# Kernel optimization log

Measured on AMD Instinct MI355X. Metric: run time of the kernel, lower is better.

Reference implementation:

```python
import jax, jax.numpy as jnp
import numpy as np

N_NODES = 100000
N_EDGES = 1600000
N_GRAPHS = 1024
HID = 32
EPS = 1e-5


def gcn_conv(x, W, b, row, col):
    # PyG GCNConv: h = x @ W, then symmetric-normalized scatter-add over
    # edges (self-loops already included in row/col).
    h = x @ W  # [N, out]
    deg = jax.ops.segment_sum(jnp.ones_like(col, dtype=h.dtype), col, num_segments=N_NODES)
    dinv = jnp.where(deg > 0, jax.lax.rsqrt(jnp.maximum(deg, 1.0)), 0.0)
    norm = dinv[row] * dinv[col]  # [E+N]
    msg = h[row] * norm[:, None]
    out = jax.ops.segment_sum(msg, col, num_segments=N_NODES)
    return out + b


def graph_norm(x, batch, weight, bias, mean_scale):
    # PyG GraphNorm: per-graph mean/var with learnable mean scale.
    ones = jnp.ones((x.shape[0], 1), dtype=x.dtype)
    cnt = jnp.maximum(jax.ops.segment_sum(ones, batch, num_segments=N_GRAPHS), 1.0)  # [G,1]
    mean = jax.ops.segment_sum(x, batch, num_segments=N_GRAPHS) / cnt
    out = x - mean[batch] * mean_scale
    var = jax.ops.segment_sum(out * out, batch, num_segments=N_GRAPHS) / cnt
    std = jnp.sqrt(var + EPS)
    return weight * out / std[batch] + bias


def setup_inputs() -> dict:
    key = jax.random.key(0)
    ks = jax.random.split(key, 16)
    x = jax.random.normal(ks[0], (N_NODES, 3), dtype=jnp.float32)
    edge_index = jax.random.randint(ks[1], (2, N_EDGES), 0, N_NODES, dtype=jnp.int64)
    batch = jnp.sort(jax.random.randint(ks[2], (N_NODES,), 0, N_GRAPHS, dtype=jnp.int64))
    def lin_init(k, fan_in, shape):
        bound = 1.0 / np.sqrt(fan_in)
        return jax.random.uniform(k, shape, jnp.float32, -bound, bound)
    params = {
        "W1": lin_init(ks[3], 3, (3, HID)), "b1": lin_init(ks[4], 3, (HID,)),
        "W2": lin_init(ks[5], HID, (HID, HID)), "b2": lin_init(ks[6], HID, (HID,)),
        "W3": lin_init(ks[7], HID, (HID, HID)), "b3": lin_init(ks[8], HID, (HID,)),
        "g1": jnp.ones((HID,)), "be1": jnp.zeros((HID,)), "ms1": jnp.ones((HID,)),
        "g2": jnp.ones((HID,)), "be2": jnp.zeros((HID,)), "ms2": jnp.ones((HID,)),
        "g3": jnp.ones((HID,)), "be3": jnp.zeros((HID,)), "ms3": jnp.ones((HID,)),
        "Wl": lin_init(ks[9], HID, (HID, 3)), "bl": lin_init(ks[10], HID, (3,)),
    }
    return {"x": x, "edge_index": edge_index, "batch": batch, **params}


def reference(x, edge_index, batch, W1, b1, W2, b2, W3, b3,
              g1, be1, ms1, g2, be2, ms2, g3, be3, ms3, Wl, bl):
    # Eval mode: dropouts / feature mask / edge dropout are identity.
    loops = jnp.arange(N_NODES, dtype=edge_index.dtype)
    row = jnp.concatenate([edge_index[0], loops])
    col = jnp.concatenate([edge_index[1], loops])

    x1 = jax.nn.relu(graph_norm(gcn_conv(x, W1, b1, row, col), batch, g1, be1, ms1))
    h2 = graph_norm(gcn_conv(x1, W2, b2, row, col), batch, g2, be2, ms2)
    x2 = jax.nn.relu(h2 + x1)
    h3 = graph_norm(gcn_conv(x2, W3, b3, row, col), batch, g3, be3, ms3)
    x3 = jax.nn.relu(h3 + x2)

    pooled = jax.ops.segment_sum(x3, batch, num_segments=N_GRAPHS)  # [G, HID]
    counts = jax.ops.segment_sum(jnp.ones((N_NODES,), jnp.float32), batch, num_segments=N_GRAPHS)
    pooled = pooled / jnp.maximum(counts, 1.0)[:, None]
    return pooled @ Wl + bl  # [G, 3]
```

## Files before the change

kernel.cpp:

```cpp
#include <hip/hip_runtime.h>
#include <hip/hip_fp16.h>


#define NN 100000
#define NE 1600000
#define NG 1024
#define HD 32
#define EPSV 1e-5f

#define FILL_PASSES 4
#define FILL_BLOCKS 2048
#define NPP ((NN + FILL_PASSES - 1) / FILL_PASSES)

__global__ __launch_bounds__(256) void k_bound(const int* __restrict__ batch,
                                               int* __restrict__ gstart) {
    int v = blockIdx.x * 256 + threadIdx.x;
    if (v >= NN) return;
    int b = batch[v];
    int bp = (v > 0) ? batch[v - 1] : -1;
    for (int g = bp + 1; g <= b; g++) gstart[g] = v;
    if (v == NN - 1)
        for (int g = b + 1; g <= NG; g++) gstart[g] = NN;
}

__global__ __launch_bounds__(256) void k_count(const int* __restrict__ col,
                                               int* __restrict__ deg) {
    int e = blockIdx.x * 256 + threadIdx.x;
    if (e < NE) atomicAdd(&deg[col[e]], 1);
}

__global__ __launch_bounds__(256) void k_alloc(const int* __restrict__ deg,
                                               int* __restrict__ start,
                                               float* __restrict__ dinv,
                                               int* __restrict__ counter) {
    int v = blockIdx.x * 256 + threadIdx.x;
    int lane = threadIdx.x & 63;
    int d = (v < NN) ? (deg[v] + 1) : 0;
    int incl = d;
    #pragma unroll
    for (int off = 1; off < 64; off <<= 1) {
        int n = __shfl_up(incl, off);
        if (lane >= off) incl += n;
    }
    int total = __shfl(incl, 63);
    int base = 0;
    if (lane == 63) base = atomicAdd(counter, total);
    base = __shfl(base, 63);
    if (v < NN) {
        start[v] = base + incl - d;
        dinv[v] = rsqrtf((float)d);
    }
}

__global__ __launch_bounds__(256) void k_fill(const int* __restrict__ row,
                                              const int* __restrict__ col,
                                              const int* __restrict__ start,
                                              int* __restrict__ fill,
                                              int* __restrict__ csr_src) {
    const int total = NE + NN;
    const int chunk = (total + FILL_BLOCKS - 1) / FILL_BLOCKS;
    int c0 = blockIdx.x * chunk;
    int c1 = min(c0 + chunk, total);
    for (int pass = 0; pass < FILL_PASSES; pass++) {
        int lo = pass * NPP;
        int hi = lo + NPP;
        for (int e = c0 + threadIdx.x; e < c1; e += 256) {
            int r, c;
            if (e < NE) { r = row[e]; c = col[e]; }
            else        { r = e - NE; c = r; }
            if (c >= lo && c < hi) {
                int pos = start[c] + atomicAdd(&fill[c], 1);
                csr_src[pos] = r;
            }
        }
    }
}

template <int K>
__global__ __launch_bounds__(256) void k_premul(const float* __restrict__ xin,
                                                const float* __restrict__ W,
                                                const float* __restrict__ dinv,
                                                __half* __restrict__ hs) {
    __shared__ float sW[K * HD];
    for (int i = threadIdx.x; i < K * HD; i += 256) sW[i] = W[i];
    __syncthreads();
    int t = blockIdx.x * 256 + threadIdx.x;
    int v = t >> 2, o = t & 3;
    if (v >= NN) return;
    const float* xv = xin + (size_t)v * K;
    float acc[8] = {0.f, 0.f, 0.f, 0.f, 0.f, 0.f, 0.f, 0.f};
    #pragma unroll
    for (int k = 0; k < K; k++) {
        float xk = xv[k];
        #pragma unroll
        for (int j = 0; j < 8; j++) acc[j] += xk * sW[k * HD + o * 8 + j];
    }
    float dv = dinv[v];
    __half2 h[4];
    #pragma unroll
    for (int j = 0; j < 4; j++)
        h[j] = __floats2half2_rn(dv * acc[2 * j], dv * acc[2 * j + 1]);
    *reinterpret_cast<float4*>(hs + (size_t)v * HD + o * 8) = *reinterpret_cast<float4*>(h);
}

__global__ __launch_bounds__(256) void k_gather(const __half* __restrict__ hs,
                                                const int* __restrict__ csr_src,
                                                const int* __restrict__ start,
                                                const int* __restrict__ deg,
                                                const float* __restrict__ dinv,
                                                const float* __restrict__ bias,
                                                float* __restrict__ outb) {
    int wid = (blockIdx.x * 256 + threadIdx.x) >> 6;
    if (wid >= NN) return;
    int lane = threadIdx.x & 63;
    int q = lane & 3;
    int es = lane >> 2;
    int s = start[wid], d = deg[wid] + 1;
    float acc[8] = {0.f, 0.f, 0.f, 0.f, 0.f, 0.f, 0.f, 0.f};

    bool a0 = (es < d);
    bool a1 = (es + 16 < d);
    int src0 = a0 ? csr_src[s + es] : 0;
    int src1 = a1 ? csr_src[s + es + 16] : 0;
    float4 raw0 = *reinterpret_cast<const float4*>(hs + (size_t)src0 * HD + q * 8);
    float4 raw1 = *reinterpret_cast<const float4*>(hs + (size_t)src1 * HD + q * 8);
    float m0 = a0 ? 1.f : 0.f;
    float m1 = a1 ? 1.f : 0.f;
    {
        const __half2* hp = reinterpret_cast<const __half2*>(&raw0);
        #pragma unroll
        for (int j = 0; j < 4; j++) {
            float2 f2 = __half22float2(hp[j]);
            acc[2 * j]     += m0 * f2.x;
            acc[2 * j + 1] += m0 * f2.y;
        }
    }
    {
        const __half2* hp = reinterpret_cast<const __half2*>(&raw1);
        #pragma unroll
        for (int j = 0; j < 4; j++) {
            float2 f2 = __half22float2(hp[j]);
            acc[2 * j]     += m1 * f2.x;
            acc[2 * j + 1] += m1 * f2.y;
        }
    }
    for (int i = es + 32; i < d; i += 16) {
        int src = csr_src[s + i];
        float4 raw = *reinterpret_cast<const float4*>(hs + (size_t)src * HD + q * 8);
        const __half2* hp = reinterpret_cast<const __half2*>(&raw);
        #pragma unroll
        for (int j = 0; j < 4; j++) {
            float2 f2 = __half22float2(hp[j]);
            acc[2 * j]     += f2.x;
            acc[2 * j + 1] += f2.y;
        }
    }
    #pragma unroll
    for (int off = 4; off < 64; off <<= 1) {
        #pragma unroll
        for (int j = 0; j < 8; j++) acc[j] += __shfl_xor(acc[j], off);
    }
    if (es == 0) {
        float dv = dinv[wid];
        float4 w0, w1;
        w0.x = bias[q * 8 + 0] + dv * acc[0];
        w0.y = bias[q * 8 + 1] + dv * acc[1];
        w0.z = bias[q * 8 + 2] + dv * acc[2];
        w0.w = bias[q * 8 + 3] + dv * acc[3];
        w1.x = bias[q * 8 + 4] + dv * acc[4];
        w1.y = bias[q * 8 + 5] + dv * acc[5];
        w1.z = bias[q * 8 + 6] + dv * acc[6];
        w1.w = bias[q * 8 + 7] + dv * acc[7];
        float* op = outb + (size_t)wid * HD + q * 8;
        *reinterpret_cast<float4*>(op)     = w0;
        *reinterpret_cast<float4*>(op + 4) = w1;
    }
}

template <bool RES, bool POOL>
__global__ __launch_bounds__(256) void k_gnorm(const float* __restrict__ o,
                                               const int* __restrict__ gstart,
                                               const float* __restrict__ gamma,
                                               const float* __restrict__ beta,
                                               const float* __restrict__ msc,
                                               const float* __restrict__ xprev,
                                               float* __restrict__ xout,
                                               const float* __restrict__ Wl,
                                               const float* __restrict__ bl,
                                               float* __restrict__ outf) {
    int g = blockIdx.x;
    int s = gstart[g], e = gstart[g + 1];
    int f = threadIdx.x & 31, nl = threadIdx.x >> 5;
    float as = 0.f, aq = 0.f;
    for (int v = s + nl; v < e; v += 8) {
        float xv = o[(size_t)v * HD + f];
        as += xv;
        aq += xv * xv;
    }
    __shared__ float ls[256], lq[256];
    __shared__ float sA[HD], sB[HD];
    ls[threadIdx.x] = as;
    lq[threadIdx.x] = aq;
    __syncthreads();
    if (threadIdx.x < HD) {
        float ss = 0.f, qq = 0.f;
        #pragma unroll
        for (int k = 0; k < 8; k++) { ss += ls[k * 32 + f]; qq += lq[k * 32 + f]; }
        float inv = 1.f / fmaxf((float)(e - s), 1.f);
        float m = ss * inv, mq = qq * inv, ms = msc[f];
        float var = mq - m * m * ms * (2.f - ms);
        float A = gamma[f] * rsqrtf(var + EPSV);
        sA[f] = A;
        sB[f] = beta[f] - A * m * ms;
    }
    __syncthreads();
    float A = sA[f], B = sB[f];
    float pool = 0.f;
    for (int v = s + nl; v < e; v += 8) {
        float xv = o[(size_t)v * HD + f];
        float y = A * xv + B;
        if (RES) y += xprev[(size_t)v * HD + f];
        y = fmaxf(y, 0.f);
        xout[(size_t)v * HD + f] = y;
        if (POOL) pool += y;
    }
    if (POOL) {
        __syncthreads();
        ls[threadIdx.x] = pool;
        __syncthreads();
        if (threadIdx.x < HD) {
            float ss = 0.f;
            #pragma unroll
            for (int k = 0; k < 8; k++) ss += ls[k * 32 + f];
            lq[f] = ss / fmaxf((float)(e - s), 1.f);
        }
        __syncthreads();
        if (threadIdx.x < 3) {
            float acc = bl[threadIdx.x];
            #pragma unroll
            for (int f2 = 0; f2 < HD; f2++) acc += lq[f2] * Wl[f2 * 3 + threadIdx.x];
            outf[g * 3 + threadIdx.x] = acc;
        }
    }
}

extern "C" void kernel_launch(void* const* d_in, const int* in_sizes, int n_in,
                              void* d_out, int out_size, void* d_ws, size_t ws_size,
                              hipStream_t stream) {
    const float* x     = (const float*)d_in[0];
    const int*   ei    = (const int*)d_in[1];
    const int*   batch = (const int*)d_in[2];
    const float* W1 = (const float*)d_in[3];
    const float* b1 = (const float*)d_in[4];
    const float* W2 = (const float*)d_in[5];
    const float* b2 = (const float*)d_in[6];
    const float* W3 = (const float*)d_in[7];
    const float* b3 = (const float*)d_in[8];
    const float* g1 = (const float*)d_in[9];
    const float* be1 = (const float*)d_in[10];
    const float* ms1 = (const float*)d_in[11];
    const float* g2 = (const float*)d_in[12];
    const float* be2 = (const float*)d_in[13];
    const float* ms2 = (const float*)d_in[14];
    const float* g3 = (const float*)d_in[15];
    const float* be3 = (const float*)d_in[16];
    const float* ms3 = (const float*)d_in[17];
    const float* Wl = (const float*)d_in[18];
    const float* bl = (const float*)d_in[19];
    float* out = (float*)d_out;

    const int* row = ei;
    const int* col = ei + NE;

    char* ws = (char*)d_ws;
    size_t off = 0;
    int*   fill    = (int*)(ws + off);   off += (size_t)NN * 4;
    int*   deg     = (int*)(ws + off);   off += (size_t)NN * 4;
    int*   counter = (int*)(ws + off);   off += 16;
    size_t zero_bytes = off;
    int*   start   = (int*)(ws + off);   off += (size_t)NN * 4;
    float* dinv    = (float*)(ws + off); off += (size_t)NN * 4;
    int*   gstart  = (int*)(ws + off);   off += (size_t)(NG + 4) * 4;
    int*   csr_src = (int*)(ws + off);   off += (size_t)(NE + NN) * 4;
    __half* bufH   = (__half*)(ws + off); off += (size_t)NN * HD * 2;
    float* bufO    = (float*)(ws + off); off += (size_t)NN * HD * 4;
    float* bufX    = (float*)(ws + off); off += (size_t)NN * HD * 4;
    (void)ws_size; (void)in_sizes; (void)n_in; (void)out_size;

    hipMemsetAsync(ws, 0, zero_bytes, stream);

    const int nb_n   = (NN + 255) / 256;
    const int nb_e   = (NE + 255) / 256;
    const int nb_no  = (NN * 4 + 255) / 256;
    const int nb_gw  = (NN * 64 + 255) / 256;

    k_bound<<<nb_n, 256, 0, stream>>>(batch, gstart);
    k_count<<<nb_e, 256, 0, stream>>>(col, deg);
    k_alloc<<<nb_n, 256, 0, stream>>>(deg, start, dinv, counter);
    k_fill <<<FILL_BLOCKS, 256, 0, stream>>>(row, col, start, fill, csr_src);

    k_premul<3><<<nb_no, 256, 0, stream>>>(x, W1, dinv, bufH);
    k_gather<<<nb_gw, 256, 0, stream>>>(bufH, csr_src, start, deg, dinv, b1, bufO);
    k_gnorm<false, false><<<NG, 256, 0, stream>>>(bufO, gstart, g1, be1, ms1,
                                                  nullptr, bufX, nullptr, nullptr, nullptr);

    k_premul<HD><<<nb_no, 256, 0, stream>>>(bufX, W2, dinv, bufH);
    k_gather<<<nb_gw, 256, 0, stream>>>(bufH, csr_src, start, deg, dinv, b2, bufO);
    k_gnorm<true, false><<<NG, 256, 0, stream>>>(bufO, gstart, g2, be2, ms2,
                                                 bufX, bufX, nullptr, nullptr, nullptr);

    k_premul<HD><<<nb_no, 256, 0, stream>>>(bufX, W3, dinv, bufH);
    k_gather<<<nb_gw, 256, 0, stream>>>(bufH, csr_src, start, deg, dinv, b3, bufO);
    k_gnorm<true, true><<<NG, 256, 0, stream>>>(bufO, gstart, g3, be3, ms3,
                                                bufX, bufX, Wl, bl, out);
}
```

Baseline: 431.1 us.

## Partition CSR fill by source and destination ranges and slice gather by source

The CSR fill kernel now makes 16 passes over its edge chunk, one for each source-range and destination-range pair, so that the CSR entries within each destination segment are grouped by source node. The gather kernel splits its first two loads into four source-range slices, issuing masked loads per slice in the hope that concurrent waves touch a narrower region of hs and hit cache more often. The cost is four times more fill passes over the edges, and four times as many loads in the gather's first stage, most of them redundant masked loads of a dummy row.

After: 455.1 us. 1.06x slower.

```diff
diff --git a/kernel.cpp b/kernel.cpp
--- a/kernel.cpp
+++ b/kernel.cpp
@@ -8,9 +8,14 @@
 #define HD 32
 #define EPSV 1e-5f
 
-#define FILL_PASSES 4
+#define FP_S 4
+#define FP_D 4
 #define FILL_BLOCKS 2048
-#define NPP ((NN + FILL_PASSES - 1) / FILL_PASSES)
+#define SRC_RANGE ((NN + FP_S - 1) / FP_S)
+#define DST_RANGE ((NN + FP_D - 1) / FP_D)
+
+#define GP 4
+#define GSLICE ((NN + GP - 1) / GP)
 
 __global__ __launch_bounds__(256) void k_bound(const int* __restrict__ batch,
                                                int* __restrict__ gstart) {
@@ -61,16 +66,18 @@
     const int chunk = (total + FILL_BLOCKS - 1) / FILL_BLOCKS;
     int c0 = blockIdx.x * chunk;
     int c1 = min(c0 + chunk, total);
-    for (int pass = 0; pass < FILL_PASSES; pass++) {
-        int lo = pass * NPP;
-        int hi = lo + NPP;
-        for (int e = c0 + threadIdx.x; e < c1; e += 256) {
-            int r, c;
-            if (e < NE) { r = row[e]; c = col[e]; }
-            else        { r = e - NE; c = r; }
-            if (c >= lo && c < hi) {
-                int pos = start[c] + atomicAdd(&fill[c], 1);
-                csr_src[pos] = r;
+    for (int sp = 0; sp < FP_S; sp++) {
+        int slo = sp * SRC_RANGE, shi = slo + SRC_RANGE;
+        for (int dp = 0; dp < FP_D; dp++) {
+            int dlo = dp * DST_RANGE, dhi = dlo + DST_RANGE;
+            for (int e = c0 + threadIdx.x; e < c1; e += 256) {
+                int r, c;
+                if (e < NE) { r = row[e]; c = col[e]; }
+                else        { r = e - NE; c = r; }
+                if (r >= slo && r < shi && c >= dlo && c < dhi) {
+                    int pos = start[c] + atomicAdd(&fill[c], 1);
+                    csr_src[pos] = r;
+                }
             }
         }
     }
@@ -116,32 +123,40 @@
     int q = lane & 3;
     int es = lane >> 2;
     int s = start[wid], d = deg[wid] + 1;
-    float acc[8] = {0.f, 0.f, 0.f, 0.f, 0.f, 0.f, 0.f, 0.f};
-
     bool a0 = (es < d);
     bool a1 = (es + 16 < d);
     int src0 = a0 ? csr_src[s + es] : 0;
     int src1 = a1 ? csr_src[s + es + 16] : 0;
-    float4 raw0 = *reinterpret_cast<const float4*>(hs + (size_t)src0 * HD + q * 8);
-    float4 raw1 = *reinterpret_cast<const float4*>(hs + (size_t)src1 * HD + q * 8);
-    float m0 = a0 ? 1.f : 0.f;
-    float m1 = a1 ? 1.f : 0.f;
-    {
-        const __half2* hp = reinterpret_cast<const __half2*>(&raw0);
-        #pragma unroll
-        for (int j = 0; j < 4; j++) {
-            float2 f2 = __half22float2(hp[j]);
-            acc[2 * j]     += m0 * f2.x;
-            acc[2 * j + 1] += m0 * f2.y;
-        }
-    }
-    {
-        const __half2* hp = reinterpret_cast<const __half2*>(&raw1);
-        #pragma unroll
-        for (int j = 0; j < 4; j++) {
-            float2 f2 = __half22float2(hp[j]);
-            acc[2 * j]     += m1 * f2.x;
-            acc[2 * j + 1] += m1 * f2.y;
+    float acc[8] = {0.f, 0.f, 0.f, 0.f, 0.f, 0.f, 0.f, 0.f};
+
+    #pragma unroll
+    for (int p = 0; p < GP; p++) {
+        int slo = p * GSLICE, shi = slo + GSLICE;
+        bool r0 = a0 && (src0 >= slo) && (src0 < shi);
+        bool r1 = a1 && (src1 >= slo) && (src1 < shi);
+        int t0 = r0 ? src0 : slo;
+        int t1 = r1 ? src1 : slo;
+        float4 raw0 = *reinterpret_cast<const float4*>(hs + (size_t)t0 * HD + q * 8);
+        float4 raw1 = *reinterpret_cast<const float4*>(hs + (size_t)t1 * HD + q * 8);
+        float m0 = r0 ? 1.f : 0.f;
+        float m1 = r1 ? 1.f : 0.f;
+        {
+            const __half2* hp = reinterpret_cast<const __half2*>(&raw0);
+            #pragma unroll
+            for (int j = 0; j < 4; j++) {
+                float2 f2 = __half22float2(hp[j]);
+                acc[2 * j]     += m0 * f2.x;
+                acc[2 * j + 1] += m0 * f2.y;
+            }
+        }
+        {
+            const __half2* hp = reinterpret_cast<const __half2*>(&raw1);
+            #pragma unroll
+            for (int j = 0; j < 4; j++) {
+                float2 f2 = __half22float2(hp[j]);
+                acc[2 * j]     += m1 * f2.x;
+                acc[2 * j + 1] += m1 * f2.y;
+            }
         }
     }
     for (int i = es + 32; i < d; i += 16) {
```

## Partition degree count and CSR fill by destination range per XCD

Applied to the files above, without the earlier changes.

Both the degree-count and CSR-fill kernels now give each block a destination-node range chosen by blockIdx modulo 8, on the assumption that consecutive blocks are dispatched round-robin across the 8 XCDs. Atomics to deg and fill for a given node range therefore stay within one XCD's L2 instead of bouncing across dies. The fill kernel drops its four sequential passes in favour of this spatial split, and the count kernel adopts the same scheme. In exchange every edge index is read eight times, once per range group, and the benefit depends on the hardware's block-to-XCD mapping.

Measured after the change: 427.5 us. About the same (-0.8%).

```diff
diff --git a/kernel.cpp b/kernel.cpp
--- a/kernel.cpp
+++ b/kernel.cpp
@@ -8,9 +8,10 @@
 #define HD 32
 #define EPSV 1e-5f
 
-#define FILL_PASSES 4
+#define NXCD 8
+#define DR8 ((NN + NXCD - 1) / NXCD)
 #define FILL_BLOCKS 2048
-#define NPP ((NN + FILL_PASSES - 1) / FILL_PASSES)
+#define COUNT_BLOCKS 2048
 
 __global__ __launch_bounds__(256) void k_bound(const int* __restrict__ batch,
                                                int* __restrict__ gstart) {
@@ -25,8 +26,16 @@
 
 __global__ __launch_bounds__(256) void k_count(const int* __restrict__ col,
                                                int* __restrict__ deg) {
-    int e = blockIdx.x * 256 + threadIdx.x;
-    if (e < NE) atomicAdd(&deg[col[e]], 1);
+    int grp = blockIdx.x & (NXCD - 1);
+    int bin = blockIdx.x / NXCD;
+    const int NB = COUNT_BLOCKS / NXCD;
+    int lo = grp * DR8, hi = min(lo + DR8, NN);
+    const int chunk = (NE + NB - 1) / NB;
+    int c0 = bin * chunk, c1 = min(c0 + chunk, NE);
+    for (int e = c0 + threadIdx.x; e < c1; e += 256) {
+        int c = col[e];
+        if (c >= lo && c < hi) atomicAdd(&deg[c], 1);
+    }
 }
 
 __global__ __launch_bounds__(256) void k_alloc(const int* __restrict__ deg,
@@ -57,21 +66,20 @@
                                               const int* __restrict__ start,
                                               int* __restrict__ fill,
                                               int* __restrict__ csr_src) {
+    int grp = blockIdx.x & (NXCD - 1);
+    int bin = blockIdx.x / NXCD;
+    const int NB = FILL_BLOCKS / NXCD;
+    int lo = grp * DR8, hi = min(lo + DR8, NN);
     const int total = NE + NN;
-    const int chunk = (total + FILL_BLOCKS - 1) / FILL_BLOCKS;
-    int c0 = blockIdx.x * chunk;
-    int c1 = min(c0 + chunk, total);
-    for (int pass = 0; pass < FILL_PASSES; pass++) {
-        int lo = pass * NPP;
-        int hi = lo + NPP;
-        for (int e = c0 + threadIdx.x; e < c1; e += 256) {
-            int r, c;
-            if (e < NE) { r = row[e]; c = col[e]; }
-            else        { r = e - NE; c = r; }
-            if (c >= lo && c < hi) {
-                int pos = start[c] + atomicAdd(&fill[c], 1);
-                csr_src[pos] = r;
-            }
+    const int chunk = (total + NB - 1) / NB;
+    int c0 = bin * chunk, c1 = min(c0 + chunk, total);
+    for (int e = c0 + threadIdx.x; e < c1; e += 256) {
+        int r, c;
+        if (e < NE) { r = row[e]; c = col[e]; }
+        else        { r = e - NE; c = r; }
+        if (c >= lo && c < hi) {
+            int pos = start[c] + atomicAdd(&fill[c], 1);
+            csr_src[pos] = r;
         }
     }
 }
@@ -290,12 +298,11 @@
     hipMemsetAsync(ws, 0, zero_bytes, stream);
 
     const int nb_n   = (NN + 255) / 256;
-    const int nb_e   = (NE + 255) / 256;
     const int nb_no  = (NN * 4 + 255) / 256;
     const int nb_gw  = (NN * 64 + 255) / 256;
 
     k_bound<<<nb_n, 256, 0, stream>>>(batch, gstart);
-    k_count<<<nb_e, 256, 0, stream>>>(col, deg);
+    k_count<<<COUNT_BLOCKS, 256, 0, stream>>>(col, deg);
     k_alloc<<<nb_n, 256, 0, stream>>>(deg, start, dinv, counter);
     k_fill <<<FILL_BLOCKS, 256, 0, stream>>>(row, col, start, fill, csr_src);
 
```
